# Kernel tuning notes

Hardware: AMD Instinct MI355X
Metric: run time of the kernel (lower is better)

Reference implementation:

```python
import jax, jax.numpy as jnp
import numpy as np

LEAK = 0.2  # LeakyReLU alpha

def setup_inputs() -> dict:
    key = jax.random.key(0)
    k1, k2, k3, k4 = jax.random.split(key, 4)
    B, N, D, H = 4, 1024, 64, 64
    qs = jax.random.normal(k1, (B, N, D), dtype=jnp.float32)
    ks = jax.random.normal(k2, (B, N, D), dtype=jnp.float32)
    vs = jax.random.normal(k3, (B, N, D), dtype=jnp.float32)
    W = jax.random.normal(k4, (3 * D, H), dtype=jnp.float32) * 0.05  # Dense kernel on concat(q,k,q-k)
    b = jnp.zeros((H,), dtype=jnp.float32)
    a = jnp.ones((H,), dtype=jnp.float32)
    return {"qs": qs, "ks": ks, "vs": vs, "W": W, "b": b, "a": a}

def reference(qs, ks, vs, W, b, a):
    D = qs.shape[-1]
    norm = 1.0 / jnp.sqrt(jnp.asarray(D, dtype=qs.dtype))
    # Dense on concat(q, k, q-k) splits as q@(Wq+Wd) + k@(Wk-Wd) + b,
    # avoiding the O(N^2 * 3D) concat tensor (same math as TF concat->Dense).
    Wq, Wk, Wd = W[:D], W[D:2 * D], W[2 * D:]
    hq = qs @ (Wq + Wd)            # [B, N, H]  query-side term
    hk = ks @ (Wk - Wd)            # [B, N, H]  key-side term
    h = hq[:, :, None, :] + hk[:, None, :, :] + b   # [B, N, N, H]
    h = jnp.where(h > 0, h, LEAK * h)               # LeakyReLU(0.2)
    scores = jnp.einsum('bijh,h->bij', h, a) * norm # [B, N, N]
    att = jax.nn.softmax(scores, axis=-1)
    return jnp.matmul(att, vs)                      # [B, N, D]
```

## Files before the change

kernel.cpp:

```cpp
#include <hip/hip_runtime.h>
#include <math.h>

#define LOG2E 1.4426950408889634f
typedef __attribute__((ext_vector_type(2))) _Float16 h2v;
typedef __attribute__((ext_vector_type(8))) _Float16 f16x8;
typedef __attribute__((ext_vector_type(4))) float f32x4;

static __device__ __forceinline__ unsigned pkrtz_u32(float lo, float hi) {
  auto p = __builtin_amdgcn_cvt_pkrtz(lo, hi);
  unsigned u; __builtin_memcpy(&u, &p, 4); return u;
}
static __device__ __forceinline__ h2v habs2(h2v x) {
  unsigned u; __builtin_memcpy(&u, &x, 4);
  u &= 0x7FFF7FFFu;
  h2v r; __builtin_memcpy(&r, &u, 4); return r;
}
static __device__ __forceinline__ h2v u2h(unsigned u) {
  h2v r; __builtin_memcpy(&r, &u, 4); return r;
}


__global__ __launch_bounds__(256) void prep_kernel(
    const float* __restrict__ qs, const float* __restrict__ ks,
    const float* __restrict__ W, const float* __restrict__ bias,
    const float* __restrict__ a,
    unsigned* __restrict__ hq2, uint4* __restrict__ khT4,
    float* __restrict__ Dj, unsigned* __restrict__ abd2) {
  __shared__ __align__(16) float wcomb[64][68];
  __shared__ __align__(16) float xin[64][68];
  const int blk = blockIdx.x;
  const bool qpart = blk < 64;
  const int r0 = (qpart ? blk : blk - 64) * 64;
  const int t = threadIdx.x;
  const float* src = qpart ? qs : ks;
  if (blk == 0 && t < 32) {
    abd2[t] = pkrtz_u32(0.05f * a[2 * t], 0.05f * a[2 * t + 1]);
  }
  for (int rep = 0; rep < 16; ++rep) {
    int e = rep * 256 + t;
    int row = e >> 6, col = e & 63;
    float wd = W[(128 + row) * 64 + col];
    float wm = qpart ? (W[row * 64 + col] + wd)
                     : (W[(64 + row) * 64 + col] - wd);
    wcomb[row][col] = wm;
    xin[row][col] = src[(r0 + row) * 64 + col];
  }
  __syncthreads();
  const int r = t >> 2;
  const int h0 = (t & 3) << 4;
  float acc[16];
#pragma unroll
  for (int k = 0; k < 16; ++k) acc[k] = 0.f;
#pragma unroll 8
  for (int d = 0; d < 64; ++d) {
    float xv = xin[r][d];
#pragma unroll
    for (int c = 0; c < 4; ++c) {
      float4 w4 = *(const float4*)&wcomb[d][h0 + (c << 2)];
      acc[c * 4 + 0] = fmaf(xv, w4.x, acc[c * 4 + 0]);
      acc[c * 4 + 1] = fmaf(xv, w4.y, acc[c * 4 + 1]);
      acc[c * 4 + 2] = fmaf(xv, w4.z, acc[c * 4 + 2]);
      acc[c * 4 + 3] = fmaf(xv, w4.w, acc[c * 4 + 3]);
    }
  }
  int grow = r0 + r;
  if (qpart) {
    unsigned pr[8];
#pragma unroll
    for (int i = 0; i < 8; ++i) pr[i] = pkrtz_u32(acc[2 * i], acc[2 * i + 1]);
    uint4* dst = (uint4*)&hq2[grow * 32 + (t & 3) * 8];
    dst[0] = make_uint4(pr[0], pr[1], pr[2], pr[3]);
    dst[1] = make_uint4(pr[4], pr[5], pr[6], pr[7]);
  } else {
    int bidx = grow >> 10;
    int j = grow & 1023;
    float val[16];
    float part = 0.f;
#pragma unroll
    for (int k = 0; k < 16; ++k) {
      val[k] = acc[k] + bias[h0 + k];
      part += a[h0 + k] * val[k];
    }
    part += __shfl_xor(part, 1);
    part += __shfl_xor(part, 2);
    if ((t & 3) == 0) Dj[bidx * 1024 + j] = 0.075f * part;
    unsigned pr[8];
#pragma unroll
    for (int i = 0; i < 8; ++i) pr[i] = pkrtz_u32(val[2 * i], val[2 * i + 1]);
    const int h4a = (t & 3) * 2;
    khT4[(bidx * 8 + h4a) * 1024 + j]     = make_uint4(pr[0], pr[1], pr[2], pr[3]);
    khT4[(bidx * 8 + h4a + 1) * 1024 + j] = make_uint4(pr[4], pr[5], pr[6], pr[7]);
  }
}

__global__ __launch_bounds__(256) void vpack_kernel(
    const float* __restrict__ vs, uint4* __restrict__ vfrag) {
  const int unit = blockIdx.x;
  const int b = unit >> 5, kstep = unit & 31;
  const int t = threadIdx.x;
  const int lane = t & 63, ntile = t >> 6;
  const int j0 = kstep * 32 + (lane >> 4) * 8;
  const int d = ntile * 16 + (lane & 15);
  const float* vb = vs + b * 1024 * 64;
  unsigned pr[4];
#pragma unroll
  for (int i = 0; i < 4; ++i)
    pr[i] = pkrtz_u32(vb[(j0 + 2 * i) * 64 + d], vb[(j0 + 2 * i + 1) * 64 + d]);
  vfrag[((b * 32 + kstep) * 4 + ntile) * 64 + lane] =
      make_uint4(pr[0], pr[1], pr[2], pr[3]);
}

__global__ __launch_bounds__(256) void attn11_kernel(
    const uint4* __restrict__ vfrag,
    const unsigned* __restrict__ hq2, const uint4* __restrict__ khT4,
    const float* __restrict__ Dj, const unsigned* __restrict__ abd2,
    float* __restrict__ out) {
  __shared__ __align__(16) unsigned p2u[4 * 520];
  __shared__ __align__(16) float ob[16 * 64];
  __shared__ __align__(16) unsigned q2lds[4 * 32];
  __shared__ __align__(16) unsigned ab2lds[32];
  __shared__ float redm[4][4];
  __shared__ float redl[4][4];

  const int t = threadIdx.x;
  const int lane = t & 63;
  const int w = t >> 6;
  const int b = blockIdx.y;
  const int rowbase = blockIdx.x * 4;
  const int growbase = b * 1024 + rowbase;

  const uint4* kh_b = khT4 + (size_t)b * 8 * 1024;
  const uint4* vf_b = vfrag + (size_t)b * 32 * 4 * 64;

  if (t < 128) q2lds[t] = hq2[growbase * 32 + t];
  if (t >= 128 && t < 160) ab2lds[t - 128] = abd2[t - 128];
  __syncthreads();

  const int jloc = w * 256 + lane * 4;
  float4 d4 = *(const float4*)(Dj + b * 1024 + jloc);

  float s[4][4];
#pragma unroll
  for (int r = 0; r < 4; ++r)
#pragma unroll
    for (int c = 0; c < 4; ++c) s[r][c] = 0.f;

  uint4 kc0 = kh_b[jloc], kc1 = kh_b[jloc + 1], kc2 = kh_b[jloc + 2],
        kc3 = kh_b[jloc + 3];
#pragma unroll 1
  for (int it = 0; it < 8; ++it) {
    const int nx = (it < 7) ? it + 1 : it;
    uint4 kn0 = kh_b[nx * 1024 + jloc];
    uint4 kn1 = kh_b[nx * 1024 + jloc + 1];
    uint4 kn2 = kh_b[nx * 1024 + jloc + 2];
    uint4 kn3 = kh_b[nx * 1024 + jloc + 3];
    uint4 abq = *(const uint4*)&ab2lds[it * 4];
    const unsigned abu[4] = {abq.x, abq.y, abq.z, abq.w};
    const unsigned kcu[4][4] = {{kc0.x, kc0.y, kc0.z, kc0.w},
                                {kc1.x, kc1.y, kc1.z, kc1.w},
                                {kc2.x, kc2.y, kc2.z, kc2.w},
                                {kc3.x, kc3.y, kc3.z, kc3.w}};
#pragma unroll
    for (int r = 0; r < 4; ++r) {
      uint4 qq = *(const uint4*)&q2lds[r * 32 + it * 4];
      const unsigned qu[4] = {qq.x, qq.y, qq.z, qq.w};
#pragma unroll
      for (int u = 0; u < 4; ++u) {
        h2v qh = u2h(qu[u]);
        h2v a2 = u2h(abu[u]);
#pragma unroll
        for (int c = 0; c < 4; ++c) {
          h2v x = habs2(qh + u2h(kcu[c][u]));
          s[r][c] = __builtin_amdgcn_fdot2(a2, x, s[r][c], false);
        }
      }
    }
    kc0 = kn0; kc1 = kn1; kc2 = kn2; kc3 = kn3;
  }
#pragma unroll
  for (int r = 0; r < 4; ++r) {
    s[r][0] += d4.x; s[r][1] += d4.y; s[r][2] += d4.z; s[r][3] += d4.w;
  }

#pragma unroll
  for (int r = 0; r < 4; ++r) {
    float m = fmaxf(fmaxf(s[r][0], s[r][1]), fmaxf(s[r][2], s[r][3]));
#pragma unroll
    for (int off = 32; off >= 1; off >>= 1) m = fmaxf(m, __shfl_xor(m, off));
    if (lane == 0) redm[r][w] = m;
  }
  __syncthreads();
  float mx[4];
#pragma unroll
  for (int r = 0; r < 4; ++r) {
    float4 rm = *(const float4*)&redm[r][0];
    mx[r] = fmaxf(fmaxf(rm.x, rm.y), fmaxf(rm.z, rm.w));
  }
#pragma unroll
  for (int r = 0; r < 4; ++r) {
    float p0 = __builtin_amdgcn_exp2f((s[r][0] - mx[r]) * LOG2E);
    float p1 = __builtin_amdgcn_exp2f((s[r][1] - mx[r]) * LOG2E);
    float p2 = __builtin_amdgcn_exp2f((s[r][2] - mx[r]) * LOG2E);
    float p3 = __builtin_amdgcn_exp2f((s[r][3] - mx[r]) * LOG2E);
    *(uint2*)&p2u[r * 520 + (jloc >> 1)] =
        make_uint2(pkrtz_u32(p0, p1), pkrtz_u32(p2, p3));
    float ps = (p0 + p1) + (p2 + p3);
#pragma unroll
    for (int off = 32; off >= 1; off >>= 1) ps += __shfl_xor(ps, off);
    if (lane == 0) redl[r][w] = ps;
  }
  __syncthreads();

  f32x4 acc[4];
#pragma unroll
  for (int nt = 0; nt < 4; ++nt) acc[nt] = (f32x4){0.f, 0.f, 0.f, 0.f};
  const int arow = (lane & 3) * 520;
  const int kgr = (lane >> 4) * 8;
#pragma unroll 2
  for (int ks = 0; ks < 8; ++ks) {
    const int j0 = w * 256 + ks * 32;
    uint4 au = *(const uint4*)&p2u[arow + ((j0 + kgr) >> 1)];
    f16x8 af; __builtin_memcpy(&af, &au, 16);
    const int gks = j0 >> 5;
#pragma unroll
    for (int nt = 0; nt < 4; ++nt) {
      uint4 bu = vf_b[(gks * 4 + nt) * 64 + lane];
      f16x8 bf; __builtin_memcpy(&bf, &bu, 16);
      acc[nt] = __builtin_amdgcn_mfma_f32_16x16x32_f16(af, bf, acc[nt], 0, 0, 0);
    }
  }

  if (lane < 16) {
#pragma unroll
    for (int nt = 0; nt < 4; ++nt)
#pragma unroll
      for (int rg = 0; rg < 4; ++rg)
        ob[(w * 4 + rg) * 64 + nt * 16 + lane] = acc[nt][rg];
  }
  __syncthreads();
  {
    int r = t >> 6, d = t & 63;
    float ax = 0.f;
#pragma unroll
    for (int wv = 0; wv < 4; ++wv) ax += ob[(wv * 4 + r) * 64 + d];
    float4 rl = *(const float4*)&redl[r][0];
    float inv = 1.f / ((rl.x + rl.y) + (rl.z + rl.w));
    out[(growbase + r) * 64 + d] = ax * inv;
  }
}

extern "C" void kernel_launch(void* const* d_in, const int* in_sizes, int n_in,
                              void* d_out, int out_size, void* d_ws, size_t ws_size,
                              hipStream_t stream) {
  const float* qs = (const float*)d_in[0];
  const float* ks = (const float*)d_in[1];
  const float* vs = (const float*)d_in[2];
  const float* W  = (const float*)d_in[3];
  const float* bi = (const float*)d_in[4];
  const float* a  = (const float*)d_in[5];
  float* out = (float*)d_out;
  unsigned* hq2   = (unsigned*)d_ws;
  uint4*    khT4  = (uint4*)((char*)d_ws + 524288);
  float*    Dj    = (float*)((char*)d_ws + 1048576);
  unsigned* abd2  = (unsigned*)((char*)d_ws + 1064960);
  uint4*    vfrag = (uint4*)((char*)d_ws + 1065216);
  prep_kernel<<<128, 256, 0, stream>>>(qs, ks, W, bi, a, hq2, khT4, Dj, abd2);
  vpack_kernel<<<128, 256, 0, stream>>>(vs, vfrag);
  attn11_kernel<<<dim3(256, 4), 256, 0, stream>>>(vfrag, hq2, khT4, Dj, abd2, out);
}
```

Baseline: 38.14 us.

## Fuse V packing into prep kernel and drop softmax max barrier via per-wave rescale

```diff
diff --git a/kernel.cpp b/kernel.cpp
--- a/kernel.cpp
+++ b/kernel.cpp
@@ -22,20 +22,38 @@
 
 __global__ __launch_bounds__(256) void prep_kernel(
     const float* __restrict__ qs, const float* __restrict__ ks,
+    const float* __restrict__ vs,
     const float* __restrict__ W, const float* __restrict__ bias,
     const float* __restrict__ a,
     unsigned* __restrict__ hq2, uint4* __restrict__ khT4,
-    float* __restrict__ Dj, unsigned* __restrict__ abd2) {
+    float* __restrict__ Dj, unsigned* __restrict__ abd2,
+    uint4* __restrict__ vfrag) {
   __shared__ __align__(16) float wcomb[64][68];
   __shared__ __align__(16) float xin[64][68];
   const int blk = blockIdx.x;
+  const int t = threadIdx.x;
+
+  if (blk >= 128) {
+    const int unit = blk - 128;
+    const int b = unit >> 5, kstep = unit & 31;
+    const int lane = t & 63, ntile = t >> 6;
+    const int j0 = kstep * 32 + (lane >> 4) * 8;
+    const int d = ntile * 16 + (lane & 15);
+    const float* vb = vs + b * 1024 * 64;
+    unsigned pr[4];
+#pragma unroll
+    for (int i = 0; i < 4; ++i)
+      pr[i] = pkrtz_u32(vb[(j0 + 2 * i) * 64 + d], vb[(j0 + 2 * i + 1) * 64 + d]);
+    vfrag[((b * 32 + kstep) * 4 + ntile) * 64 + lane] =
+        make_uint4(pr[0], pr[1], pr[2], pr[3]);
+    return;
+  }
+
   const bool qpart = blk < 64;
   const int r0 = (qpart ? blk : blk - 64) * 64;
-  const int t = threadIdx.x;
   const float* src = qpart ? qs : ks;
-  if (blk == 0 && t < 32) {
+  if (blk == 0 && t < 32)
     abd2[t] = pkrtz_u32(0.05f * a[2 * t], 0.05f * a[2 * t + 1]);
-  }
   for (int rep = 0; rep < 16; ++rep) {
     int e = rep * 256 + t;
     int row = e >> 6, col = e & 63;
@@ -93,31 +111,14 @@
   }
 }
 
-__global__ __launch_bounds__(256) void vpack_kernel(
-    const float* __restrict__ vs, uint4* __restrict__ vfrag) {
-  const int unit = blockIdx.x;
-  const int b = unit >> 5, kstep = unit & 31;
-  const int t = threadIdx.x;
-  const int lane = t & 63, ntile = t >> 6;
-  const int j0 = kstep * 32 + (lane >> 4) * 8;
-  const int d = ntile * 16 + (lane & 15);
-  const float* vb = vs + b * 1024 * 64;
-  unsigned pr[4];
-#pragma unroll
-  for (int i = 0; i < 4; ++i)
-    pr[i] = pkrtz_u32(vb[(j0 + 2 * i) * 64 + d], vb[(j0 + 2 * i + 1) * 64 + d]);
-  vfrag[((b * 32 + kstep) * 4 + ntile) * 64 + lane] =
-      make_uint4(pr[0], pr[1], pr[2], pr[3]);
-}
-
-__global__ __launch_bounds__(256) void attn11_kernel(
+__global__ __launch_bounds__(256) void attn12_kernel(
     const uint4* __restrict__ vfrag,
     const unsigned* __restrict__ hq2, const uint4* __restrict__ khT4,
     const float* __restrict__ Dj, const unsigned* __restrict__ abd2,
     float* __restrict__ out) {
   __shared__ __align__(16) unsigned p2u[4 * 520];
   __shared__ __align__(16) float ob[16 * 64];
-  __shared__ __align__(16) unsigned q2lds[4 * 32];
+  __shared__ __align__(16) unsigned q2lds[128];
   __shared__ __align__(16) unsigned ab2lds[32];
   __shared__ float redm[4][4];
   __shared__ float redl[4][4];
@@ -145,63 +146,67 @@
 #pragma unroll
     for (int c = 0; c < 4; ++c) s[r][c] = 0.f;
 
-  uint4 kc0 = kh_b[jloc], kc1 = kh_b[jloc + 1], kc2 = kh_b[jloc + 2],
-        kc3 = kh_b[jloc + 3];
-#pragma unroll 1
-  for (int it = 0; it < 8; ++it) {
-    const int nx = (it < 7) ? it + 1 : it;
-    uint4 kn0 = kh_b[nx * 1024 + jloc];
-    uint4 kn1 = kh_b[nx * 1024 + jloc + 1];
-    uint4 kn2 = kh_b[nx * 1024 + jloc + 2];
-    uint4 kn3 = kh_b[nx * 1024 + jloc + 3];
+  auto SCORE = [&](const uint4 (&K)[4], int it) {
     uint4 abq = *(const uint4*)&ab2lds[it * 4];
-    const unsigned abu[4] = {abq.x, abq.y, abq.z, abq.w};
-    const unsigned kcu[4][4] = {{kc0.x, kc0.y, kc0.z, kc0.w},
-                                {kc1.x, kc1.y, kc1.z, kc1.w},
-                                {kc2.x, kc2.y, kc2.z, kc2.w},
-                                {kc3.x, kc3.y, kc3.z, kc3.w}};
+    unsigned abu[4] = {abq.x, abq.y, abq.z, abq.w};
+    unsigned ku[4][4] = {{K[0].x, K[0].y, K[0].z, K[0].w},
+                         {K[1].x, K[1].y, K[1].z, K[1].w},
+                         {K[2].x, K[2].y, K[2].z, K[2].w},
+                         {K[3].x, K[3].y, K[3].z, K[3].w}};
 #pragma unroll
     for (int r = 0; r < 4; ++r) {
       uint4 qq = *(const uint4*)&q2lds[r * 32 + it * 4];
-      const unsigned qu[4] = {qq.x, qq.y, qq.z, qq.w};
+      unsigned qu[4] = {qq.x, qq.y, qq.z, qq.w};
 #pragma unroll
       for (int u = 0; u < 4; ++u) {
         h2v qh = u2h(qu[u]);
         h2v a2 = u2h(abu[u]);
 #pragma unroll
         for (int c = 0; c < 4; ++c) {
-          h2v x = habs2(qh + u2h(kcu[c][u]));
+          h2v x = habs2(qh + u2h(ku[c][u]));
           s[r][c] = __builtin_amdgcn_fdot2(a2, x, s[r][c], false);
         }
       }
     }
-    kc0 = kn0; kc1 = kn1; kc2 = kn2; kc3 = kn3;
+  };
+
+  uint4 kA[4], kB[4];
+#pragma unroll
+  for (int c = 0; c < 4; ++c) kA[c] = kh_b[jloc + c];
+#pragma unroll
+  for (int c = 0; c < 4; ++c) kB[c] = kh_b[1024 + jloc + c];
+#pragma unroll 1
+  for (int it2 = 0; it2 < 4; ++it2) {
+    const int itA = 2 * it2, itB = 2 * it2 + 1;
+    const int nA = (itA + 2 < 8) ? itA + 2 : itA;
+    const int nB = (itB + 2 < 8) ? itB + 2 : itB;
+    SCORE(kA, itA);
+#pragma unroll
+    for (int c = 0; c < 4; ++c) kA[c] = kh_b[nA * 1024 + jloc + c];
+    SCORE(kB, itB);
+#pragma unroll
+    for (int c = 0; c < 4; ++c) kB[c] = kh_b[nB * 1024 + jloc + c];
   }
 #pragma unroll
   for (int r = 0; r < 4; ++r) {
     s[r][0] += d4.x; s[r][1] += d4.y; s[r][2] += d4.z; s[r][3] += d4.w;
   }
 
+  float mw[4];
 #pragma unroll
   for (int r = 0; r < 4; ++r) {
     float m = fmaxf(fmaxf(s[r][0], s[r][1]), fmaxf(s[r][2], s[r][3]));
 #pragma unroll
     for (int off = 32; off >= 1; off >>= 1) m = fmaxf(m, __shfl_xor(m, off));
+    mw[r] = m;
     if (lane == 0) redm[r][w] = m;
   }
-  __syncthreads();
-  float mx[4];
-#pragma unroll
-  for (int r = 0; r < 4; ++r) {
-    float4 rm = *(const float4*)&redm[r][0];
-    mx[r] = fmaxf(fmaxf(rm.x, rm.y), fmaxf(rm.z, rm.w));
-  }
-#pragma unroll
-  for (int r = 0; r < 4; ++r) {
-    float p0 = __builtin_amdgcn_exp2f((s[r][0] - mx[r]) * LOG2E);
-    float p1 = __builtin_amdgcn_exp2f((s[r][1] - mx[r]) * LOG2E);
-    float p2 = __builtin_amdgcn_exp2f((s[r][2] - mx[r]) * LOG2E);
-    float p3 = __builtin_amdgcn_exp2f((s[r][3] - mx[r]) * LOG2E);
+#pragma unroll
+  for (int r = 0; r < 4; ++r) {
+    float p0 = __builtin_amdgcn_exp2f((s[r][0] - mw[r]) * LOG2E);
+    float p1 = __builtin_amdgcn_exp2f((s[r][1] - mw[r]) * LOG2E);
+    float p2 = __builtin_amdgcn_exp2f((s[r][2] - mw[r]) * LOG2E);
+    float p3 = __builtin_amdgcn_exp2f((s[r][3] - mw[r]) * LOG2E);
     *(uint2*)&p2u[r * 520 + (jloc >> 1)] =
         make_uint2(pkrtz_u32(p0, p1), pkrtz_u32(p2, p3));
     float ps = (p0 + p1) + (p2 + p3);
@@ -230,12 +235,21 @@
     }
   }
 
+  float4 rmv[1];
+  float eww[4];
+#pragma unroll
+  for (int r = 0; r < 4; ++r) {
+    float4 rm = *(const float4*)&redm[r][0];
+    float M = fmaxf(fmaxf(rm.x, rm.y), fmaxf(rm.z, rm.w));
+    float mwv = (w == 0) ? rm.x : (w == 1) ? rm.y : (w == 2) ? rm.z : rm.w;
+    eww[r] = __builtin_amdgcn_exp2f((mwv - M) * LOG2E);
+  }
   if (lane < 16) {
 #pragma unroll
     for (int nt = 0; nt < 4; ++nt)
 #pragma unroll
       for (int rg = 0; rg < 4; ++rg)
-        ob[(w * 4 + rg) * 64 + nt * 16 + lane] = acc[nt][rg];
+        ob[(w * 4 + rg) * 64 + nt * 16 + lane] = acc[nt][rg] * eww[rg];
   }
   __syncthreads();
   {
@@ -243,9 +257,14 @@
     float ax = 0.f;
 #pragma unroll
     for (int wv = 0; wv < 4; ++wv) ax += ob[(wv * 4 + r) * 64 + d];
+    float4 rm = *(const float4*)&redm[r][0];
+    float M = fmaxf(fmaxf(rm.x, rm.y), fmaxf(rm.z, rm.w));
     float4 rl = *(const float4*)&redl[r][0];
-    float inv = 1.f / ((rl.x + rl.y) + (rl.z + rl.w));
-    out[(growbase + r) * 64 + d] = ax * inv;
+    float lt = rl.x * __builtin_amdgcn_exp2f((rm.x - M) * LOG2E) +
+               rl.y * __builtin_amdgcn_exp2f((rm.y - M) * LOG2E) +
+               rl.z * __builtin_amdgcn_exp2f((rm.z - M) * LOG2E) +
+               rl.w * __builtin_amdgcn_exp2f((rm.w - M) * LOG2E);
+    out[(growbase + r) * 64 + d] = ax / lt;
   }
 }
 
@@ -264,7 +283,7 @@
   float*    Dj    = (float*)((char*)d_ws + 1048576);
   unsigned* abd2  = (unsigned*)((char*)d_ws + 1064960);
   uint4*    vfrag = (uint4*)((char*)d_ws + 1065216);
-  prep_kernel<<<128, 256, 0, stream>>>(qs, ks, W, bi, a, hq2, khT4, Dj, abd2);
-  vpack_kernel<<<128, 256, 0, stream>>>(vs, vfrag);
-  attn11_kernel<<<dim3(256, 4), 256, 0, stream>>>(vfrag, hq2, khT4, Dj, abd2, out);
-}
+  prep_kernel<<<256, 256, 0, stream>>>(qs, ks, vs, W, bi, a, hq2, khT4, Dj,
+                                       abd2, vfrag);
+  attn12_kernel<<<dim3(256, 4), 256, 0, stream>>>(vfrag, hq2, khT4, Dj, abd2, out);
+}
```

After: 57.28 us. 1.5x slower.
